# Kernel tuning notes

Measured on AMD Instinct MI355X. Metric: run time of the kernel, lower is better.

The kernel has to match this reference:

```python
import jax, jax.numpy as jnp
import numpy as np

N = 10000      # nodes
E = 160000     # edges
F_IN = 128     # input_feature
G = 64         # graphs in batch
NC = 10        # num_classes
H1, H2, H3 = 1000, 700, 200


def _xavier(k, fi, fo):
    lim = float(np.sqrt(6.0 / (fi + fo)))
    return jax.random.uniform(k, (fi, fo), jnp.float32, -lim, lim)


def setup_inputs() -> dict:
    key = jax.random.key(0)
    ks = jax.random.split(key, 8)
    x = jax.random.normal(ks[0], (N, F_IN), jnp.float32)
    edge_index = jax.random.randint(ks[1], (2, E), 0, N)
    batch = jnp.sort(jax.random.randint(ks[2], (N,), 0, G))
    return {
        "x": x,
        "edge_index": edge_index,
        "batch": batch,
        "W1": _xavier(ks[3], F_IN, H1), "b1": jnp.zeros((H1,), jnp.float32),
        "W2": _xavier(ks[4], H1, H2),   "b2": jnp.zeros((H2,), jnp.float32),
        "W3": _xavier(ks[5], H2, H3),   "b3": jnp.zeros((H3,), jnp.float32),
        "Wl": _xavier(ks[6], H3, NC),   "bl": jnp.zeros((NC,), jnp.float32),
    }


def _gcn_conv(x, W, b, src, dst, dinv):
    # GCNConv: h = xW; out_i = sum_{j->i} d_j^-1/2 d_i^-1/2 h_j + d_i^-1 h_i + b
    h = x @ W
    coef = dinv[src] * dinv[dst]                      # [E]
    agg = jax.ops.segment_sum(h[src] * coef[:, None], dst, num_segments=N)
    agg = agg + h * (dinv * dinv)[:, None]            # self-loop term
    return agg + b


def reference(x, edge_index, batch, W1, b1, W2, b2, W3, b3, Wl, bl):
    src, dst = edge_index[0], edge_index[1]
    # degree with self-loops (edge weight 1), computed on target nodes
    deg = jax.ops.segment_sum(jnp.ones((E,), x.dtype), dst, num_segments=N) + 1.0
    dinv = jax.lax.rsqrt(deg)

    h = jax.nn.relu(_gcn_conv(x, W1, b1, src, dst, dinv))
    h = jax.nn.relu(_gcn_conv(h, W2, b2, src, dst, dinv))
    h = jax.nn.relu(_gcn_conv(h, W3, b3, src, dst, dinv))

    # global_mean_pool over graph ids
    s = jax.ops.segment_sum(h, batch, num_segments=G)
    cnt = jax.ops.segment_sum(jnp.ones((N,), h.dtype), batch, num_segments=G)
    pooled = s / jnp.maximum(cnt, 1.0)[:, None]

    # dropout is identity in eval mode
    return pooled @ Wl + bl
```

## Files before the change

### kernel.cpp

```cpp
#include <hip/hip_runtime.h>
#include <hip/hip_bf16.h>
#include <stdint.h>


#define SLOT 64

__device__ __forceinline__ uint16_t f2b(float f) {
    union { float f; uint32_t u; } v; v.f = f;
    return (uint16_t)((v.u + 0x7fffu + ((v.u >> 16) & 1u)) >> 16);
}
__device__ __forceinline__ float blo(uint32_t u) { union { uint32_t u; float f; } v; v.u = u << 16; return v.f; }
__device__ __forceinline__ float bhi(uint32_t u) { union { uint32_t u; float f; } v; v.u = u & 0xffff0000u; return v.f; }

__global__ void k_scatter(const int* __restrict__ src, const int* __restrict__ dst,
                          int* __restrict__ cursor, int* __restrict__ slots, int E) {
    int e = blockIdx.x * blockDim.x + threadIdx.x;
    if (e < E) {
        int s = src[e], d = dst[e];
        int pos = atomicAdd(&cursor[d], 1);
        if (pos < SLOT) slots[d * SLOT + pos] = s;
    }
}
__global__ void k_dinv(const int* __restrict__ deg, float* __restrict__ dinv, int N) {
    int i = blockIdx.x * blockDim.x + threadIdx.x;
    if (i < N) dinv[i] = rsqrtf((float)deg[i] + 1.0f);
}

__global__ void k_prep(const float* __restrict__ W1, const float* __restrict__ W2,
                       const float* __restrict__ W3,
                       uint16_t* __restrict__ T1, uint16_t* __restrict__ T2,
                       uint16_t* __restrict__ T3,
                       const float* __restrict__ b1, const float* __restrict__ b2,
                       const float* __restrict__ b3,
                       float* __restrict__ p1, float* __restrict__ p2,
                       float* __restrict__ p3,
                       const float* __restrict__ x, uint16_t* __restrict__ xb,
                       int F, int H1, int H2, int H3,
                       int Fp, int H1p, int H2p, int H3p, int n8) {
    __shared__ float tile[32][33];
    int z = blockIdx.z;
    if (z < 3) {
        const float* W; uint16_t* T; int K, Nn, Kp, Np;
        if (z == 0)      { W = W1; T = T1; K = F;  Nn = H1; Kp = Fp;  Np = H1p; }
        else if (z == 1) { W = W2; T = T2; K = H1; Nn = H2; Kp = H1p; Np = H2p; }
        else             { W = W3; T = T3; K = H2; Nn = H3; Kp = H2p; Np = H3p; }
        if ((int)blockIdx.x * 32 >= Kp || (int)blockIdx.y * 32 >= Np) return;
        int k0 = blockIdx.x * 32, n0 = blockIdx.y * 32;
        int tx = threadIdx.x, ty = threadIdx.y;
        for (int i = ty; i < 32; i += 8) {
            int k = k0 + i, n = n0 + tx;
            tile[i][tx] = (k < K && n < Nn) ? W[(size_t)k * Nn + n] : 0.f;
        }
        __syncthreads();
        for (int i = ty; i < 32; i += 8) {
            int n = n0 + i, k = k0 + tx;
            T[(size_t)n * Kp + k] = f2b(tile[tx][i]);
        }
    } else {
        int id = (blockIdx.y * gridDim.x + blockIdx.x) * 256 + threadIdx.y * 32 + threadIdx.x;
        if (z == 3) {
            if (id < H1p) p1[id] = (id < H1) ? b1[id] : 0.f;
            else if (id < H1p + H2p) { int k = id - H1p; p2[k] = (k < H2) ? b2[k] : 0.f; }
            else if (id < H1p + H2p + H3p) { int k = id - H1p - H2p; p3[k] = (k < H3) ? b3[k] : 0.f; }
        } else {
            if (id < n8) {
                const float4* x4 = (const float4*)x;
                float4 a = x4[2 * id], b = x4[2 * id + 1];
                uint4 o;
                o.x = (uint32_t)f2b(a.x) | ((uint32_t)f2b(a.y) << 16);
                o.y = (uint32_t)f2b(a.z) | ((uint32_t)f2b(a.w) << 16);
                o.z = (uint32_t)f2b(b.x) | ((uint32_t)f2b(b.y) << 16);
                o.w = (uint32_t)f2b(b.z) | ((uint32_t)f2b(b.w) << 16);
                ((uint4*)xb)[id] = o;
            }
        }
    }
}

__global__ __launch_bounds__(256) void k_agg_panel(
    const uint16_t* __restrict__ in, uint16_t* __restrict__ out,
    const int* __restrict__ deg_, const int* __restrict__ slots,
    const float* __restrict__ dinv, const float* __restrict__ bias,
    int N, int Hc, int pc, int P, int relu) {
    int slotg = blockIdx.x & 7;
    int panel = slotg % P;
    int seg   = slotg / P;
    int nseg  = 8 / P;
    int segLen = (N + nseg - 1) / nseg;
    int wave = threadIdx.x >> 6, lane = threadIdx.x & 63;
    int half = lane >> 5, sub = lane & 31;
    int item = (blockIdx.x >> 3) * 128 + wave * 32 + sub;
    int rel = item / pc;
    if (rel >= segLen) return;
    int node = seg * segLen + rel;
    if (node >= N) return;
    int j = panel * pc + (item - rel * pc);
    int deg = deg_[node];
    if (deg > SLOT) deg = SLOT;
    int dh = (deg + 1) >> 1;
    int e  = half ? dh : 0;
    int eE = half ? deg : dh;
    int base = node * SLOT;
    float dv = dinv[node];
    const uint4* in4 = (const uint4*)in;
    float a[8] = {0.f, 0.f, 0.f, 0.f, 0.f, 0.f, 0.f, 0.f};
    if (half == 0) {
        float self = dv * dv;
        uint4 v = in4[(size_t)node * Hc + j];
        a[0] = self * blo(v.x); a[1] = self * bhi(v.x);
        a[2] = self * blo(v.y); a[3] = self * bhi(v.y);
        a[4] = self * blo(v.z); a[5] = self * bhi(v.z);
        a[6] = self * blo(v.w); a[7] = self * bhi(v.w);
    }
    for (; e + 2 <= eE; e += 2) {
        int s0 = slots[base + e], s1 = slots[base + e + 1];
        uint4 h0 = in4[(size_t)s0 * Hc + j];
        uint4 h1 = in4[(size_t)s1 * Hc + j];
        float c0 = dinv[s0] * dv, c1 = dinv[s1] * dv;
        a[0] += c0 * blo(h0.x); a[1] += c0 * bhi(h0.x);
        a[2] += c0 * blo(h0.y); a[3] += c0 * bhi(h0.y);
        a[4] += c0 * blo(h0.z); a[5] += c0 * bhi(h0.z);
        a[6] += c0 * blo(h0.w); a[7] += c0 * bhi(h0.w);
        a[0] += c1 * blo(h1.x); a[1] += c1 * bhi(h1.x);
        a[2] += c1 * blo(h1.y); a[3] += c1 * bhi(h1.y);
        a[4] += c1 * blo(h1.z); a[5] += c1 * bhi(h1.z);
        a[6] += c1 * blo(h1.w); a[7] += c1 * bhi(h1.w);
    }
    if (e < eE) {
        int s0 = slots[base + e];
        uint4 h = in4[(size_t)s0 * Hc + j];
        float c = dinv[s0] * dv;
        a[0] += c * blo(h.x); a[1] += c * bhi(h.x);
        a[2] += c * blo(h.y); a[3] += c * bhi(h.y);
        a[4] += c * blo(h.z); a[5] += c * bhi(h.z);
        a[6] += c * blo(h.w); a[7] += c * bhi(h.w);
    }
#pragma unroll
    for (int t = 0; t < 8; ++t) a[t] += __shfl_xor(a[t], 32, 64);
    if (half == 0) {
        if (bias) {
            const float4* b4 = (const float4*)bias;
            float4 b0 = b4[2 * j], b1 = b4[2 * j + 1];
            a[0] += b0.x; a[1] += b0.y; a[2] += b0.z; a[3] += b0.w;
            a[4] += b1.x; a[5] += b1.y; a[6] += b1.z; a[7] += b1.w;
        }
        if (relu) {
#pragma unroll
            for (int t = 0; t < 8; ++t) a[t] = fmaxf(a[t], 0.f);
        }
        uint4 o;
        o.x = (uint32_t)f2b(a[0]) | ((uint32_t)f2b(a[1]) << 16);
        o.y = (uint32_t)f2b(a[2]) | ((uint32_t)f2b(a[3]) << 16);
        o.z = (uint32_t)f2b(a[4]) | ((uint32_t)f2b(a[5]) << 16);
        o.w = (uint32_t)f2b(a[6]) | ((uint32_t)f2b(a[7]) << 16);
        ((uint4*)out)[(size_t)node * Hc + j] = o;
    }
}

__global__ __launch_bounds__(256) void k_pool_fast(
    const uint16_t* __restrict__ h, const int* __restrict__ batch,
    float* __restrict__ pooled_sum, int N, int H, int Hp) {
    int j    = threadIdx.x & 63;
    int slot = threadIdx.x >> 6;
    int Hc   = H >> 2;
    if (j >= Hc) return;
    int HcP  = Hp >> 2;
    const uint2* h2 = (const uint2*)h;
    int base = (blockIdx.x * 4 + slot) * 16;
    float a0 = 0.f, a1 = 0.f, a2 = 0.f, a3 = 0.f;
    int gcur = -1;
#pragma unroll 4
    for (int t = 0; t < 16; ++t) {
        int node = base + t;
        if (node < N) {
            int g = batch[node];
            if (g != gcur) {
                if (gcur >= 0) {
                    float* ps = &pooled_sum[(size_t)gcur * H + j * 4];
                    atomicAdd(&ps[0], a0); atomicAdd(&ps[1], a1);
                    atomicAdd(&ps[2], a2); atomicAdd(&ps[3], a3);
                }
                gcur = g; a0 = a1 = a2 = a3 = 0.f;
            }
            uint2 v = h2[(size_t)node * HcP + j];
            a0 += blo(v.x); a1 += bhi(v.x);
            a2 += blo(v.y); a3 += bhi(v.y);
        }
    }
    if (gcur >= 0) {
        float* ps = &pooled_sum[(size_t)gcur * H + j * 4];
        atomicAdd(&ps[0], a0); atomicAdd(&ps[1], a1);
        atomicAdd(&ps[2], a2); atomicAdd(&ps[3], a3);
    }
}

typedef __attribute__((ext_vector_type(8))) short short8;
typedef __attribute__((ext_vector_type(4))) float floatx4;

#define LDSP(p) ((__attribute__((address_space(3))) void*)(uintptr_t)(p))
#define GLBP(p) ((const __attribute__((address_space(1))) void*)(uintptr_t)(p))

__global__ __launch_bounds__(256) void k_gemm_bf16(
    const uint16_t* __restrict__ A, const uint16_t* __restrict__ Bt,
    const float* __restrict__ bias, void* __restrict__ Cout,
    int M, int Kp, int Np, int relu, int out_bf16) {
    __shared__ uint16_t As[128 * 64];
    __shared__ uint16_t Bs[64 * 64];
    int tid = threadIdx.x;
    int wave = tid >> 6, lane = tid & 63;
    int quad = lane >> 4, m16 = lane & 15;
    int wr = wave >> 1, wc = wave & 1;
    int row0 = blockIdx.y * 128, col0 = blockIdx.x * 64;

    int rA = tid >> 3;
    int cA = (tid & 7) ^ (rA & 7);
    const uint16_t* gA = A  + (size_t)(row0 + rA) * Kp + cA * 8;
    const uint16_t* gB = Bt + (size_t)(col0 + rA) * Kp + cA * 8;
    uint16_t* lA = As + tid * 8;
    uint16_t* lB = Bs + tid * 8;
    size_t rowStep32 = (size_t)32 * Kp;

    floatx4 acc[4][2];
#pragma unroll
    for (int i = 0; i < 4; ++i)
#pragma unroll
        for (int j = 0; j < 2; ++j) acc[i][j] = (floatx4){0.f, 0.f, 0.f, 0.f};

    const short* Ash = (const short*)As;
    const short* Bsh = (const short*)Bs;
    int swA = m16 & 7;

    for (int k0 = 0; k0 < Kp; k0 += 64) {
#pragma unroll
        for (int p = 0; p < 4; ++p)
            __builtin_amdgcn_global_load_lds(GLBP(gA + p * rowStep32), LDSP(lA + p * 2048), 16, 0, 0);
#pragma unroll
        for (int p = 0; p < 2; ++p)
            __builtin_amdgcn_global_load_lds(GLBP(gB + p * rowStep32), LDSP(lB + p * 2048), 16, 0, 0);
        gA += 64; gB += 64;
        __syncthreads();
#pragma unroll
        for (int h = 0; h < 2; ++h) {
            short8 af[4], bf[2];
            int c = h * 4 + quad;
            int pos = (c ^ swA) * 8;
#pragma unroll
            for (int i = 0; i < 4; ++i)
                af[i] = *(const short8*)&Ash[(wr * 64 + i * 16 + m16) * 64 + pos];
#pragma unroll
            for (int j = 0; j < 2; ++j)
                bf[j] = *(const short8*)&Bsh[(wc * 32 + j * 16 + m16) * 64 + pos];
#pragma unroll
            for (int i = 0; i < 4; ++i)
#pragma unroll
                for (int j = 0; j < 2; ++j)
                    acc[i][j] = __builtin_amdgcn_mfma_f32_16x16x32_bf16(af[i], bf[j], acc[i][j], 0, 0, 0);
        }
        __syncthreads();
    }

    float bv[2];
#pragma unroll
    for (int j = 0; j < 2; ++j) {
        int n = col0 + wc * 32 + j * 16 + m16;
        bv[j] = bias ? bias[n] : 0.f;
    }
#pragma unroll
    for (int i = 0; i < 4; ++i) {
        int mBase = row0 + wr * 64 + i * 16 + quad * 4;
#pragma unroll
        for (int r = 0; r < 4; ++r) {
            int m = mBase + r;
            if (m < M) {
#pragma unroll
                for (int j = 0; j < 2; ++j) {
                    int n = col0 + wc * 32 + j * 16 + m16;
                    float v = acc[i][j][r] + bv[j];
                    if (relu) v = fmaxf(v, 0.f);
                    if (out_bf16) ((uint16_t*)Cout)[(size_t)m * Np + n] = f2b(v);
                    else          ((float*)Cout)[(size_t)m * Np + n]    = v;
                }
            }
        }
    }
}

__global__ void k_classifier(const float* __restrict__ pooled_sum,
                             const int* __restrict__ batch,
                             const float* __restrict__ Wl, const float* __restrict__ bl,
                             float* __restrict__ out, int N, int H, int NC) {
    int g = blockIdx.x, c = threadIdx.x;
    int lo = 0, hi = N;
    while (lo < hi) { int mid = (lo + hi) >> 1; if (batch[mid] < g) lo = mid + 1; else hi = mid; }
    int start = lo;
    lo = start; hi = N;
    while (lo < hi) { int mid = (lo + hi) >> 1; if (batch[mid] < g + 1) lo = mid + 1; else hi = mid; }
    int end = lo;
    float scale = 1.0f / fmaxf((float)(end - start), 1.0f);
    if (c < NC) {
        float acc = 0.f;
        for (int k = 0; k < H; ++k) acc += pooled_sum[(size_t)g * H + k] * Wl[(size_t)k * NC + c];
        out[(size_t)g * NC + c] = acc * scale + bl[c];
    }
}

static inline size_t align256(size_t x) { return (x + 255) & ~(size_t)255; }
static inline int pad128(int x) { return (x + 127) & ~127; }

extern "C" void kernel_launch(void* const* d_in, const int* in_sizes, int n_in,
                              void* d_out, int out_size, void* d_ws, size_t ws_size,
                              hipStream_t stream) {
    const float* x   = (const float*)d_in[0];
    const int*   ei  = (const int*)d_in[1];
    const int*   bat = (const int*)d_in[2];
    const float* W1  = (const float*)d_in[3];
    const float* b1  = (const float*)d_in[4];
    const float* W2  = (const float*)d_in[5];
    const float* b2  = (const float*)d_in[6];
    const float* W3  = (const float*)d_in[7];
    const float* b3  = (const float*)d_in[8];
    const float* Wl  = (const float*)d_in[9];
    const float* bl  = (const float*)d_in[10];

    const int N  = in_sizes[2];
    const int E  = in_sizes[1] / 2;
    const int F  = in_sizes[0] / N;
    const int H1 = in_sizes[4];
    const int H2 = in_sizes[6];
    const int H3 = in_sizes[8];
    const int NC = in_sizes[10];
    const int G  = out_size / NC;
    const int* src = ei;
    const int* dst = ei + E;

    const int Mp  = pad128(N);
    const int Fp  = F;
    const int H1p = pad128(H1);
    const int H2p = pad128(H2);
    const int H3p = pad128(H3);

    char* p = (char*)d_ws;
    size_t off = 0;
    auto carve = [&](size_t bytes) { void* q = p + off; off += align256(bytes); return q; };
    uint16_t* xb     = (uint16_t*)carve((size_t)Mp * Fp * 2);
    uint16_t* bufA   = (uint16_t*)carve((size_t)Mp * 2048);
    uint16_t* bufB   = (uint16_t*)carve((size_t)Mp * 2048);
    uint16_t* W1t    = (uint16_t*)carve((size_t)H1p * Fp * 2);
    uint16_t* W2t    = (uint16_t*)carve((size_t)H2p * H1p * 2);
    uint16_t* W3t    = (uint16_t*)carve((size_t)H3p * H2p * 2);
    float* b1p       = (float*)carve((size_t)H1p * 4);
    float* b2p       = (float*)carve((size_t)H2p * 4);
    float* b3p       = (float*)carve((size_t)H3p * 4);
    float* dinv      = (float*)carve((size_t)N * 4);
    int*   cursor    = (int*)carve((size_t)N * 4);
    float* pooled    = (float*)carve((size_t)G * H3 * 4);
    int*   slots     = (int*)carve((size_t)N * SLOT * 4);
    (void)ws_size;

    const int nbN = (N + 255) / 256;
    const int nbE = (E + 255) / 256;

    size_t zlen = (size_t)((char*)pooled - (char*)cursor) + (size_t)G * H3 * 4;
    hipMemsetAsync(cursor, 0, zlen, stream);

    k_scatter<<<nbE, 256, 0, stream>>>(src, dst, cursor, slots, E);
    k_dinv<<<nbN, 256, 0, stream>>>(cursor, dinv, N);

    k_prep<<<dim3(32, 32, 5), dim3(32, 8), 0, stream>>>(
        W1, W2, W3, W1t, W2t, W3t, b1, b2, b3, b1p, b2p, b3p, x, xb,
        F, H1, H2, H3, Fp, H1p, H2p, H3p, N * F / 8);

    auto agg_grid = [&](int P, int pc) {
        int nseg = 8 / P;
        int segLen = (N + nseg - 1) / nseg;
        return 8 * ((segLen * pc + 127) / 128);
    };

    k_agg_panel<<<agg_grid(1, 16), 256, 0, stream>>>(
        xb, bufA, cursor, slots, dinv, nullptr, N, 16, 16, 1, 0);
    k_gemm_bf16<<<dim3(H1p / 64, Mp / 128), 256, 0, stream>>>(
        bufA, W1t, b1p, bufB, N, Fp, H1p, 1, 1);

    k_gemm_bf16<<<dim3(H2p / 64, Mp / 128), 256, 0, stream>>>(
        bufB, W2t, nullptr, bufA, N, H1p, H2p, 0, 1);
    k_agg_panel<<<agg_grid(8, 12), 256, 0, stream>>>(
        bufA, bufB, cursor, slots, dinv, b2p, N, 96, 12, 8, 1);

    k_gemm_bf16<<<dim3(H3p / 64, Mp / 128), 256, 0, stream>>>(
        bufB, W3t, nullptr, bufA, N, H2p, H3p, 0, 1);
    k_agg_panel<<<agg_grid(4, 8), 256, 0, stream>>>(
        bufA, bufB, cursor, slots, dinv, b3p, N, 32, 8, 4, 1);

    k_pool_fast<<<(N + 63) / 64, 256, 0, stream>>>(
        (const uint16_t*)bufB, bat, pooled, N, H3, H3p);
    k_classifier<<<G, 64, 0, stream>>>(pooled, bat, Wl, bl, (float*)d_out, N, H3, NC);
}
```

Before: 255.3 us.

## Add 128x128 GEMM tile, widen aggregation gather, fold dinv into prep kernel

Adds a 128x128-tile bf16 MFMA GEMM for the two large layer GEMMs, keeping the 128x64 kernel for the small third layer. This raises data reuse per block and halves the block count, but it needs H1p and H2p padded to a multiple of 128. The aggregation loop now loads neighbor indices as int4 and gathers four rows per iteration, interleaving the two half-waves in groups of four, to increase memory-level parallelism. The separate dinv kernel is merged into the prep launch as an extra z-slice to save one launch.

```diff
diff --git a/kernel.cpp b/kernel.cpp
--- a/kernel.cpp
+++ b/kernel.cpp
@@ -20,10 +20,6 @@
         int pos = atomicAdd(&cursor[d], 1);
         if (pos < SLOT) slots[d * SLOT + pos] = s;
     }
-}
-__global__ void k_dinv(const int* __restrict__ deg, float* __restrict__ dinv, int N) {
-    int i = blockIdx.x * blockDim.x + threadIdx.x;
-    if (i < N) dinv[i] = rsqrtf((float)deg[i] + 1.0f);
 }
 
 __global__ void k_prep(const float* __restrict__ W1, const float* __restrict__ W2,
@@ -35,7 +31,8 @@
                        float* __restrict__ p1, float* __restrict__ p2,
                        float* __restrict__ p3,
                        const float* __restrict__ x, uint16_t* __restrict__ xb,
-                       int F, int H1, int H2, int H3,
+                       const int* __restrict__ deg, float* __restrict__ dinv,
+                       int N, int F, int H1, int H2, int H3,
                        int Fp, int H1p, int H2p, int H3p, int n8) {
     __shared__ float tile[32][33];
     int z = blockIdx.z;
@@ -62,7 +59,7 @@
             if (id < H1p) p1[id] = (id < H1) ? b1[id] : 0.f;
             else if (id < H1p + H2p) { int k = id - H1p; p2[k] = (k < H2) ? b2[k] : 0.f; }
             else if (id < H1p + H2p + H3p) { int k = id - H1p - H2p; p3[k] = (k < H3) ? b3[k] : 0.f; }
-        } else {
+        } else if (z == 4) {
             if (id < n8) {
                 const float4* x4 = (const float4*)x;
                 float4 a = x4[2 * id], b = x4[2 * id + 1];
@@ -73,6 +70,8 @@
                 o.w = (uint32_t)f2b(b.z) | ((uint32_t)f2b(b.w) << 16);
                 ((uint4*)xb)[id] = o;
             }
+        } else {
+            if (id < N) dinv[id] = rsqrtf((float)deg[id] + 1.0f);
         }
     }
 }
@@ -97,9 +96,6 @@
     int j = panel * pc + (item - rel * pc);
     int deg = deg_[node];
     if (deg > SLOT) deg = SLOT;
-    int dh = (deg + 1) >> 1;
-    int e  = half ? dh : 0;
-    int eE = half ? deg : dh;
     int base = node * SLOT;
     float dv = dinv[node];
     const uint4* in4 = (const uint4*)in;
@@ -112,11 +108,15 @@
         a[4] = self * blo(v.z); a[5] = self * bhi(v.z);
         a[6] = self * blo(v.w); a[7] = self * bhi(v.w);
     }
-    for (; e + 2 <= eE; e += 2) {
-        int s0 = slots[base + e], s1 = slots[base + e + 1];
-        uint4 h0 = in4[(size_t)s0 * Hc + j];
-        uint4 h1 = in4[(size_t)s1 * Hc + j];
-        float c0 = dinv[s0] * dv, c1 = dinv[s1] * dv;
+    int D8 = deg & ~7;
+    for (int e = 4 * half; e < D8; e += 8) {
+        int4 q = *(const int4*)&slots[base + e];
+        uint4 h0 = in4[(size_t)q.x * Hc + j];
+        uint4 h1 = in4[(size_t)q.y * Hc + j];
+        uint4 h2 = in4[(size_t)q.z * Hc + j];
+        uint4 h3 = in4[(size_t)q.w * Hc + j];
+        float c0 = dinv[q.x] * dv, c1 = dinv[q.y] * dv;
+        float c2 = dinv[q.z] * dv, c3 = dinv[q.w] * dv;
         a[0] += c0 * blo(h0.x); a[1] += c0 * bhi(h0.x);
         a[2] += c0 * blo(h0.y); a[3] += c0 * bhi(h0.y);
         a[4] += c0 * blo(h0.z); a[5] += c0 * bhi(h0.z);
@@ -125,8 +125,18 @@
         a[2] += c1 * blo(h1.y); a[3] += c1 * bhi(h1.y);
         a[4] += c1 * blo(h1.z); a[5] += c1 * bhi(h1.z);
         a[6] += c1 * blo(h1.w); a[7] += c1 * bhi(h1.w);
-    }
-    if (e < eE) {
+        a[0] += c2 * blo(h2.x); a[1] += c2 * bhi(h2.x);
+        a[2] += c2 * blo(h2.y); a[3] += c2 * bhi(h2.y);
+        a[4] += c2 * blo(h2.z); a[5] += c2 * bhi(h2.z);
+        a[6] += c2 * blo(h2.w); a[7] += c2 * bhi(h2.w);
+        a[0] += c3 * blo(h3.x); a[1] += c3 * bhi(h3.x);
+        a[2] += c3 * blo(h3.y); a[3] += c3 * bhi(h3.y);
+        a[4] += c3 * blo(h3.z); a[5] += c3 * bhi(h3.z);
+        a[6] += c3 * blo(h3.w); a[7] += c3 * bhi(h3.w);
+    }
+    int t0 = half ? (D8 + 4 < deg ? D8 + 4 : deg) : D8;
+    int t1 = half ? deg : (D8 + 4 < deg ? D8 + 4 : deg);
+    for (int e = t0; e < t1; ++e) {
         int s0 = slots[base + e];
         uint4 h = in4[(size_t)s0 * Hc + j];
         float c = dinv[s0] * dv;
@@ -200,10 +210,93 @@
 #define LDSP(p) ((__attribute__((address_space(3))) void*)(uintptr_t)(p))
 #define GLBP(p) ((const __attribute__((address_space(1))) void*)(uintptr_t)(p))
 
-__global__ __launch_bounds__(256) void k_gemm_bf16(
+__global__ __launch_bounds__(256) void k_gemm128(
     const uint16_t* __restrict__ A, const uint16_t* __restrict__ Bt,
-    const float* __restrict__ bias, void* __restrict__ Cout,
-    int M, int Kp, int Np, int relu, int out_bf16) {
+    const float* __restrict__ bias, uint16_t* __restrict__ Cout,
+    int M, int Kp, int Np, int relu) {
+    __shared__ uint16_t As[128 * 64];
+    __shared__ uint16_t Bs[128 * 64];
+    int tid = threadIdx.x;
+    int wave = tid >> 6, lane = tid & 63;
+    int quad = lane >> 4, m16 = lane & 15;
+    int wr = wave >> 1, wc = wave & 1;
+    int row0 = blockIdx.y * 128, col0 = blockIdx.x * 128;
+
+    int rA = tid >> 3;
+    int cA = (tid & 7) ^ (rA & 7);
+    const uint16_t* gA = A  + (size_t)(row0 + rA) * Kp + cA * 8;
+    const uint16_t* gB = Bt + (size_t)(col0 + rA) * Kp + cA * 8;
+    uint16_t* lA = As + tid * 8;
+    uint16_t* lB = Bs + tid * 8;
+    size_t rowStep32 = (size_t)32 * Kp;
+
+    floatx4 acc[4][4];
+#pragma unroll
+    for (int i = 0; i < 4; ++i)
+#pragma unroll
+        for (int j = 0; j < 4; ++j) acc[i][j] = (floatx4){0.f, 0.f, 0.f, 0.f};
+
+    const short* Ash = (const short*)As;
+    const short* Bsh = (const short*)Bs;
+    int swA = m16 & 7;
+
+    for (int k0 = 0; k0 < Kp; k0 += 64) {
+#pragma unroll
+        for (int p = 0; p < 4; ++p) {
+            __builtin_amdgcn_global_load_lds(GLBP(gA + p * rowStep32), LDSP(lA + p * 2048), 16, 0, 0);
+            __builtin_amdgcn_global_load_lds(GLBP(gB + p * rowStep32), LDSP(lB + p * 2048), 16, 0, 0);
+        }
+        gA += 64; gB += 64;
+        __syncthreads();
+#pragma unroll
+        for (int h = 0; h < 2; ++h) {
+            short8 af[4], bf[4];
+            int c = h * 4 + quad;
+            int pos = (c ^ swA) * 8;
+#pragma unroll
+            for (int i = 0; i < 4; ++i)
+                af[i] = *(const short8*)&Ash[(wr * 64 + i * 16 + m16) * 64 + pos];
+#pragma unroll
+            for (int j = 0; j < 4; ++j)
+                bf[j] = *(const short8*)&Bsh[(wc * 64 + j * 16 + m16) * 64 + pos];
+#pragma unroll
+            for (int i = 0; i < 4; ++i)
+#pragma unroll
+                for (int j = 0; j < 4; ++j)
+                    acc[i][j] = __builtin_amdgcn_mfma_f32_16x16x32_bf16(af[i], bf[j], acc[i][j], 0, 0, 0);
+        }
+        __syncthreads();
+    }
+
+    float bv[4];
+#pragma unroll
+    for (int j = 0; j < 4; ++j) {
+        int n = col0 + wc * 64 + j * 16 + m16;
+        bv[j] = bias ? bias[n] : 0.f;
+    }
+#pragma unroll
+    for (int i = 0; i < 4; ++i) {
+        int mBase = row0 + wr * 64 + i * 16 + quad * 4;
+#pragma unroll
+        for (int r = 0; r < 4; ++r) {
+            int m = mBase + r;
+            if (m < M) {
+#pragma unroll
+                for (int j = 0; j < 4; ++j) {
+                    int n = col0 + wc * 64 + j * 16 + m16;
+                    float v = acc[i][j][r] + bv[j];
+                    if (relu) v = fmaxf(v, 0.f);
+                    Cout[(size_t)m * Np + n] = f2b(v);
+                }
+            }
+        }
+    }
+}
+
+__global__ __launch_bounds__(256) void k_gemm64(
+    const uint16_t* __restrict__ A, const uint16_t* __restrict__ Bt,
+    const float* __restrict__ bias, uint16_t* __restrict__ Cout,
+    int M, int Kp, int Np, int relu) {
     __shared__ uint16_t As[128 * 64];
     __shared__ uint16_t Bs[64 * 64];
     int tid = threadIdx.x;
@@ -277,8 +370,7 @@
                     int n = col0 + wc * 32 + j * 16 + m16;
                     float v = acc[i][j][r] + bv[j];
                     if (relu) v = fmaxf(v, 0.f);
-                    if (out_bf16) ((uint16_t*)Cout)[(size_t)m * Np + n] = f2b(v);
-                    else          ((float*)Cout)[(size_t)m * Np + n]    = v;
+                    Cout[(size_t)m * Np + n] = f2b(v);
                 }
             }
         }
@@ -357,18 +449,16 @@
     int*   slots     = (int*)carve((size_t)N * SLOT * 4);
     (void)ws_size;
 
-    const int nbN = (N + 255) / 256;
     const int nbE = (E + 255) / 256;
 
     size_t zlen = (size_t)((char*)pooled - (char*)cursor) + (size_t)G * H3 * 4;
     hipMemsetAsync(cursor, 0, zlen, stream);
 
     k_scatter<<<nbE, 256, 0, stream>>>(src, dst, cursor, slots, E);
-    k_dinv<<<nbN, 256, 0, stream>>>(cursor, dinv, N);
-
-    k_prep<<<dim3(32, 32, 5), dim3(32, 8), 0, stream>>>(
+
+    k_prep<<<dim3(32, 32, 6), dim3(32, 8), 0, stream>>>(
         W1, W2, W3, W1t, W2t, W3t, b1, b2, b3, b1p, b2p, b3p, x, xb,
-        F, H1, H2, H3, Fp, H1p, H2p, H3p, N * F / 8);
+        cursor, dinv, N, F, H1, H2, H3, Fp, H1p, H2p, H3p, N * F / 8);
 
     auto agg_grid = [&](int P, int pc) {
         int nseg = 8 / P;
@@ -378,16 +468,16 @@
 
     k_agg_panel<<<agg_grid(1, 16), 256, 0, stream>>>(
         xb, bufA, cursor, slots, dinv, nullptr, N, 16, 16, 1, 0);
-    k_gemm_bf16<<<dim3(H1p / 64, Mp / 128), 256, 0, stream>>>(
-        bufA, W1t, b1p, bufB, N, Fp, H1p, 1, 1);
-
-    k_gemm_bf16<<<dim3(H2p / 64, Mp / 128), 256, 0, stream>>>(
-        bufB, W2t, nullptr, bufA, N, H1p, H2p, 0, 1);
+    k_gemm128<<<dim3(H1p / 128, Mp / 128), 256, 0, stream>>>(
+        bufA, W1t, b1p, bufB, N, Fp, H1p, 1);
+
+    k_gemm128<<<dim3(H2p / 128, Mp / 128), 256, 0, stream>>>(
+        bufB, W2t, nullptr, bufA, N, H1p, H2p, 0);
     k_agg_panel<<<agg_grid(8, 12), 256, 0, stream>>>(
         bufA, bufB, cursor, slots, dinv, b2p, N, 96, 12, 8, 1);
 
-    k_gemm_bf16<<<dim3(H3p / 64, Mp / 128), 256, 0, stream>>>(
-        bufB, W3t, nullptr, bufA, N, H2p, H3p, 0, 1);
+    k_gemm64<<<dim3(H3p / 64, Mp / 128), 256, 0, stream>>>(
+        bufB, W3t, nullptr, bufA, N, H2p, H3p, 0);
     k_agg_panel<<<agg_grid(4, 8), 256, 0, stream>>>(
         bufA, bufB, cursor, slots, dinv, b3p, N, 32, 8, 4, 1);
 
```

Measured after the change: 245.4 us. 1.04x faster.
